# Kernel tuning notes

Measured on AMD Instinct MI355X. Metric: run time of the kernel, lower is better.

The kernel has to match this reference:

```python
import jax, jax.numpy as jnp
import numpy as np
import math
from jax import lax

D = 256      # d_model
H = 8        # heads
DK = D // H  # 32
P = 16       # patch size
IMG = 224
S = (IMG // P) ** 2 + 1  # 197
B = 64
EPS = 1e-5


def _ln(x, g, b):
    m = jnp.mean(x, axis=-1, keepdims=True)
    v = jnp.mean((x - m) ** 2, axis=-1, keepdims=True)
    return (x - m) / jnp.sqrt(v + EPS) * g + b


def _attn(q_in, k_in, v_in, wq, bq, wk, bk, wv, bv, wo, bo, mask):
    # torch Linear: y = x @ W^T + b
    def heads(x, w, b):
        y = x @ w.T + b
        bsz, s, _ = y.shape
        return y.reshape(bsz, s, H, DK).transpose(0, 2, 1, 3)  # [b,h,s,dk]
    q = heads(q_in, wq, bq)
    k = heads(k_in, wk, bk)
    v = heads(v_in, wv, bv)
    att = jnp.einsum('bhqd,bhkd->bhqk', q, k) / math.sqrt(DK)
    if mask is not None:
        att = jnp.where(mask == 0, -jnp.inf, att)
    att = jax.nn.softmax(att, axis=-1)
    o = jnp.einsum('bhqk,bhkd->bhqd', att, v)
    bsz, s, _ = q_in.shape  # output reshape uses q's shape (faithful to source)
    o = o.transpose(0, 2, 1, 3).reshape(bsz, s, D)
    return o @ wo.T + bo


def _patch_embed(img, conv_w, conv_b, cls, pos):
    x = lax.conv_general_dilated(img, conv_w, window_strides=(P, P),
                                 padding='VALID',
                                 dimension_numbers=('NCHW', 'OIHW', 'NCHW'))
    x = x + conv_b[None, :, None, None]
    bsz = img.shape[0]
    x = x.reshape(bsz, D, -1).transpose(0, 2, 1)  # [B,196,D]
    cls_t = jnp.broadcast_to(cls, (bsz, 1, D))
    x = jnp.concatenate([x, cls_t], axis=1)  # cls appended at END (faithful)
    return x + pos


def setup_inputs() -> dict:
    key = jax.random.key(0)
    ks = iter(jax.random.split(key, 64))
    nrm = lambda shape, s=0.02: jax.random.normal(next(ks), shape, jnp.float32) * s
    inp = {
        'enc_out': jax.random.normal(next(ks), (B, 3, IMG, IMG), jnp.float32),
        'dec_in': jax.random.normal(next(ks), (B, S, D), jnp.float32),
        'mask': jnp.ones((1, 1, S, S), jnp.int32),
        'conv_w': nrm((D, 3, P, P)),
        'conv_b': jnp.zeros((D,), jnp.float32),
        'cls': nrm((1, 1, D), 1.0),
        'pos': nrm((1, S, D), 1.0),
        'ff_w1': nrm((4 * D, D)), 'ff_b1': jnp.zeros((4 * D,), jnp.float32),
        'ff_w2': nrm((D, 4 * D)), 'ff_b2': jnp.zeros((D,), jnp.float32),
        'ln1_g': jnp.ones((D,), jnp.float32), 'ln1_b': jnp.zeros((D,), jnp.float32),
        'ln2_g': jnp.ones((D,), jnp.float32), 'ln2_b': jnp.zeros((D,), jnp.float32),
        'ln3_g': jnp.ones((D,), jnp.float32), 'ln3_b': jnp.zeros((D,), jnp.float32),
    }
    for p in ('a1', 'a2'):
        for n in ('wq', 'wk', 'wv', 'wo'):
            inp[f'{p}_{n}'] = nrm((D, D))
            inp[f'{p}_b{n[1]}'] = jnp.zeros((D,), jnp.float32)
    return inp


def reference(enc_out, dec_in, mask, conv_w, conv_b, cls, pos,
              ff_w1, ff_b1, ff_w2, ff_b2,
              ln1_g, ln1_b, ln2_g, ln2_b, ln3_g, ln3_b,
              a1_wq, a1_bq, a1_wk, a1_bk, a1_wv, a1_bv, a1_wo, a1_bo,
              a2_wq, a2_bq, a2_wk, a2_bk, a2_wv, a2_bv, a2_wo, a2_bo):
    e = _patch_embed(enc_out, conv_w, conv_b, cls, pos)  # [B,197,D]
    x = dec_in
    x = _ln(x + _attn(dec_in, dec_in, dec_in,
                      a1_wq, a1_bq, a1_wk, a1_bk, a1_wv, a1_bv, a1_wo, a1_bo,
                      None), ln1_g, ln1_b)
    # faithful: q=k=enc_out, v=dec_in, with mask
    x = _ln(x + _attn(e, e, dec_in,
                      a2_wq, a2_bq, a2_wk, a2_bk, a2_wv, a2_bv, a2_wo, a2_bo,
                      mask), ln2_g, ln2_b)
    ff = jax.nn.relu(x @ ff_w1.T + ff_b1) @ ff_w2.T + ff_b2
    x = _ln(x + ff, ln3_g, ln3_b)
    return x
```

## Files before the change

kernel.cpp:

```cpp
#include <hip/hip_runtime.h>
#include <hip/hip_bf16.h>
#include <math.h>

#define DMODEL 256
#define NH 8
#define DKH 32
#define SEQ 197
#define BATCH 64
#define NPAT 196
#define FFDIM 1024
#define KCONV 768
#define EPSLN 1e-5f
#define MROWS (BATCH * SEQ)
#define SP 224

typedef __attribute__((ext_vector_type(8))) short short8;
typedef __attribute__((ext_vector_type(4))) short short4v;
typedef __attribute__((ext_vector_type(4))) float floatx4;

__device__ inline short f2b(float f) {
  unsigned u = __float_as_uint(f);
  unsigned r = (u + 0x7FFFu + ((u >> 16) & 1u)) >> 16;
  return (short)r;
}
__device__ inline float b2f(short s) {
  return __uint_as_float(((unsigned)(unsigned short)s) << 16);
}

typedef const __attribute__((address_space(1))) unsigned int gu32;
typedef __attribute__((address_space(3))) unsigned int lu32;
__device__ __forceinline__ void gl_lds16(const void* g, void* l) {
  __builtin_amdgcn_global_load_lds((gu32*)g, (lu32*)l, 16, 0, 0);
}

__global__ __launch_bounds__(256) void convert_dec(
    const float* __restrict__ dec, short* __restrict__ dec_bf)
{
  const int ND = (MROWS * DMODEL) / 8;
  int i = blockIdx.x * 256 + threadIdx.x;
  if (i >= ND) return;
  float4 a0 = ((const float4*)dec)[i * 2];
  float4 a1 = ((const float4*)dec)[i * 2 + 1];
  short8 o;
  o[0] = f2b(a0.x); o[1] = f2b(a0.y); o[2] = f2b(a0.z); o[3] = f2b(a0.w);
  o[4] = f2b(a1.x); o[5] = f2b(a1.y); o[6] = f2b(a1.z); o[7] = f2b(a1.w);
  ((short8*)dec_bf)[i] = o;
}

__global__ __launch_bounds__(256) void prep_weights(
    const float* wq1, const float* wk1, const float* wv1,
    const float* bq1, const float* bk1, const float* bv1,
    const float* wq2, const float* wk2, const float* bq2, const float* bk2,
    const float* wv2s, const float* wo1, const float* wo2,
    const float* ffw1, const float* ffw2, const float* convw,
    short* Wqkv1, float* Bqkv1, short* Wqk2, float* Bqk2,
    short* Wv2, short* Wo1, short* Wo2, short* Wff1, short* Wff2, short* Wconv)
{
  int i = blockIdx.x * 256 + threadIdx.x;
  if (i < 65536) {
    Wqkv1[i] = f2b(wq1[i]); Wqkv1[65536 + i] = f2b(wk1[i]); Wqkv1[131072 + i] = f2b(wv1[i]);
    Wqk2[i] = f2b(wq2[i]);  Wqk2[65536 + i] = f2b(wk2[i]);
    Wv2[i] = f2b(wv2s[i]);  Wo1[i] = f2b(wo1[i]);  Wo2[i] = f2b(wo2[i]);
  }
  if (i < 262144) { Wff1[i] = f2b(ffw1[i]); Wff2[i] = f2b(ffw2[i]); }
  if (i < 196608) { Wconv[i] = f2b(convw[i]); }
  if (i < 256) {
    Bqkv1[i] = bq1[i]; Bqkv1[256 + i] = bk1[i]; Bqkv1[512 + i] = bv1[i];
    Bqk2[i] = bq2[i];  Bqk2[256 + i] = bk2[i];
  }
}

__global__ void mask_pack(const int* __restrict__ mask,
                          unsigned long long* __restrict__ bits,
                          unsigned long long* __restrict__ ones)
{
  int idx = blockIdx.x * 256 + threadIdx.x;
  if (idx >= SEQ * 4) return;
  int r = idx >> 2, w = idx & 3;
  unsigned long long bb = 0ull, oo = 0ull;
  for (int j = 0; j < 64; j++) {
    int c = w * 64 + j;
    if (c < SEQ) {
      oo |= (1ull << j);
      if (mask[r * SEQ + c] != 0) bb |= (1ull << j);
    }
  }
  bits[idx] = bb;
  ones[idx] = oo;
}

__global__ void cls_kernel(const float* __restrict__ cls, const float* __restrict__ pos,
                           short* __restrict__ e)
{
  int b = blockIdx.x, d = threadIdx.x;
  e[((size_t)b * SEQ + NPAT) * DMODEL + d] = f2b(cls[d] + pos[NPAT * DMODEL + d]);
}

__global__ __launch_bounds__(256) void gemm64(
    const short* __restrict__ A, const short* __restrict__ W,
    const float* __restrict__ bias, const short* __restrict__ res,
    float* __restrict__ outf, short* __restrict__ outb,
    int M, int N, int K, int relu)
{
  __shared__ short Al[64 * 64];
  __shared__ short Bl[64 * 64];
  int m0 = blockIdx.x * 64, n0 = blockIdx.y * 64;
  int t = threadIdx.x;
  int wave = t >> 6, lane = t & 63;
  int wm = (wave & 1) * 32, wn = (wave >> 1) * 32;
  int ml = lane & 15, quad = lane >> 4;
  int m7 = ml & 7;

  int rs = t >> 3;
  int cs = (t & 7) ^ (rs & 7);
  const short* gA0 = A + (size_t)(m0 + rs) * K + cs * 8;
  const short* gA1 = A + (size_t)(m0 + rs + 32) * K + cs * 8;
  const short* gB0 = W + (size_t)(n0 + rs) * K + cs * 8;
  const short* gB1 = W + (size_t)(n0 + rs + 32) * K + cs * 8;
  short* lA0 = &Al[t * 8];
  short* lA1 = &Al[t * 8 + 2048];
  short* lB0 = &Bl[t * 8];
  short* lB1 = &Bl[t * 8 + 2048];

  int offA[2][2], offB[2][2];
#pragma unroll
  for (int kk = 0; kk < 2; kk++)
#pragma unroll
    for (int i = 0; i < 2; i++) {
      int ra = wm + i * 16 + ml;
      offA[kk][i] = ra * 64 + (((kk * 4 + quad) ^ m7) * 8);
      int rb = wn + i * 16 + ml;
      offB[kk][i] = rb * 64 + (((kk * 4 + quad) ^ m7) * 8);
    }

  floatx4 z = {0.f, 0.f, 0.f, 0.f};
  floatx4 acc[2][2] = {{z, z}, {z, z}};

  for (int k0 = 0; k0 < K; k0 += 64) {
    __syncthreads();
    gl_lds16(gA0 + k0, lA0);
    gl_lds16(gA1 + k0, lA1);
    gl_lds16(gB0 + k0, lB0);
    gl_lds16(gB1 + k0, lB1);
    __builtin_amdgcn_s_waitcnt(0x0F70);
    __syncthreads();
#pragma unroll
    for (int kk = 0; kk < 2; kk++) {
      short8 a0 = *(const short8*)&Al[offA[kk][0]];
      short8 a1 = *(const short8*)&Al[offA[kk][1]];
      short8 b0 = *(const short8*)&Bl[offB[kk][0]];
      short8 b1 = *(const short8*)&Bl[offB[kk][1]];
      acc[0][0] = __builtin_amdgcn_mfma_f32_16x16x32_bf16(a0, b0, acc[0][0], 0, 0, 0);
      acc[0][1] = __builtin_amdgcn_mfma_f32_16x16x32_bf16(a0, b1, acc[0][1], 0, 0, 0);
      acc[1][0] = __builtin_amdgcn_mfma_f32_16x16x32_bf16(a1, b0, acc[1][0], 0, 0, 0);
      acc[1][1] = __builtin_amdgcn_mfma_f32_16x16x32_bf16(a1, b1, acc[1][1], 0, 0, 0);
    }
  }
#pragma unroll
  for (int i = 0; i < 2; i++)
#pragma unroll
    for (int j = 0; j < 2; j++)
#pragma unroll
      for (int rr = 0; rr < 4; rr++) {
        int row = m0 + wm + i * 16 + quad * 4 + rr;
        int col = n0 + wn + j * 16 + ml;
        float v = acc[i][j][rr] + bias[col];
        if (res) v += b2f(res[(size_t)row * N + col]);
        if (relu) v = fmaxf(v, 0.f);
        if (outf) outf[(size_t)row * N + col] = v;
        if (outb) outb[(size_t)row * N + col] = f2b(v);
      }
}

__global__ __launch_bounds__(256) void conv64(
    const float* __restrict__ img, const short* __restrict__ W,
    const float* __restrict__ cb, const float* __restrict__ pos,
    short* __restrict__ e)
{
  __shared__ short Al[64 * 64];
  __shared__ short Bl[64 * 64];
  int m0 = blockIdx.x * 64, n0 = blockIdx.y * 64;
  int t = threadIdx.x;
  int wave = t >> 6, lane = t & 63;
  int wm = (wave & 1) * 32, wn = (wave >> 1) * 32;
  int ml = lane & 15, quad = lane >> 4;
  int m7 = ml & 15 & 7;

  int rA = t >> 3, cg = t & 7;
  int pr_off = cg >> 1;
  int px_off = (cg & 1) * 8;
  int csw = cg ^ (rA & 7);
  const float* baseA[2];
  short* lA[2];
#pragma unroll
  for (int p = 0; p < 2; p++) {
    int m = m0 + rA + p * 32;
    int b = m / NPAT, pp = m - b * NPAT;
    int py = pp / 14, px = pp - py * 14;
    baseA[p] = img + (size_t)b * 3 * 50176 + (size_t)(py * 16) * 224 + px * 16 + px_off;
    lA[p] = &Al[(rA + p * 32) * 64 + csw * 8];
  }
  int rs = t >> 3;
  int cs = (t & 7) ^ (rs & 7);
  const short* gB0 = W + (size_t)(n0 + rs) * KCONV + cs * 8;
  const short* gB1 = W + (size_t)(n0 + rs + 32) * KCONV + cs * 8;
  short* lB0 = &Bl[t * 8];
  short* lB1 = &Bl[t * 8 + 2048];

  int offA[2][2], offB[2][2];
#pragma unroll
  for (int kk = 0; kk < 2; kk++)
#pragma unroll
    for (int i = 0; i < 2; i++) {
      int ra = wm + i * 16 + ml;
      offA[kk][i] = ra * 64 + (((kk * 4 + quad) ^ m7) * 8);
      int rb = wn + i * 16 + ml;
      offB[kk][i] = rb * 64 + (((kk * 4 + quad) ^ m7) * 8);
    }

  floatx4 z = {0.f, 0.f, 0.f, 0.f};
  floatx4 acc[2][2] = {{z, z}, {z, z}};

  for (int k0 = 0; k0 < KCONV; k0 += 64) {
    int ch = k0 >> 8;
    int rr0 = (k0 & 255) >> 4;
    __syncthreads();
    gl_lds16(gB0 + k0, lB0);
    gl_lds16(gB1 + k0, lB1);
#pragma unroll
    for (int p = 0; p < 2; p++) {
      const float* ap = baseA[p] + (size_t)ch * 50176 + (rr0 + pr_off) * 224;
      float4 a0 = *(const float4*)ap;
      float4 a1 = *(const float4*)(ap + 4);
      short8 av;
      av[0] = f2b(a0.x); av[1] = f2b(a0.y); av[2] = f2b(a0.z); av[3] = f2b(a0.w);
      av[4] = f2b(a1.x); av[5] = f2b(a1.y); av[6] = f2b(a1.z); av[7] = f2b(a1.w);
      *(short8*)lA[p] = av;
    }
    __builtin_amdgcn_s_waitcnt(0x0F70);
    __syncthreads();
#pragma unroll
    for (int kk = 0; kk < 2; kk++) {
      short8 a0 = *(const short8*)&Al[offA[kk][0]];
      short8 a1 = *(const short8*)&Al[offA[kk][1]];
      short8 b0 = *(const short8*)&Bl[offB[kk][0]];
      short8 b1 = *(const short8*)&Bl[offB[kk][1]];
      acc[0][0] = __builtin_amdgcn_mfma_f32_16x16x32_bf16(a0, b0, acc[0][0], 0, 0, 0);
      acc[0][1] = __builtin_amdgcn_mfma_f32_16x16x32_bf16(a0, b1, acc[0][1], 0, 0, 0);
      acc[1][0] = __builtin_amdgcn_mfma_f32_16x16x32_bf16(a1, b0, acc[1][0], 0, 0, 0);
      acc[1][1] = __builtin_amdgcn_mfma_f32_16x16x32_bf16(a1, b1, acc[1][1], 0, 0, 0);
    }
  }
#pragma unroll
  for (int i = 0; i < 2; i++)
#pragma unroll
    for (int j = 0; j < 2; j++)
#pragma unroll
      for (int rr = 0; rr < 4; rr++) {
        int mrow = m0 + wm + i * 16 + quad * 4 + rr;
        int b2 = mrow / NPAT, p2 = mrow - b2 * NPAT;
        int col = n0 + wn + j * 16 + ml;
        e[((size_t)b2 * SEQ + p2) * DMODEL + col] =
            f2b(acc[i][j][rr] + cb[col] + pos[p2 * DMODEL + col]);
      }
}

__global__ __launch_bounds__(256) void attn_mfma(
    const short* __restrict__ qp, int qstr,
    const short* __restrict__ kp, int kstr,
    const short* __restrict__ vp, int vstr,
    const unsigned long long* __restrict__ mbits,
    short* __restrict__ op)
{
  __shared__ short ks[SP][40];
  __shared__ short vt[DKH][SP + 8];
  __shared__ short ps[4][16][40];
  int bh = blockIdx.x;
  int b = bh >> 3, h = bh & 7;
  int t = threadIdx.x;
  int wave = t >> 6, lane = t & 63;
  int ml = lane & 15, quad = lane >> 4;

  const short* kb = kp + (size_t)b * SEQ * kstr + h * DKH;
  const short* vb = vp + (size_t)b * SEQ * vstr + h * DKH;
  for (int idx = t; idx < SEQ * 4; idx += 256) {
    int s = idx >> 2, c = (idx & 3) * 8;
    *(short8*)&ks[s][c] = *(const short8*)(kb + (size_t)s * kstr + c);
  }
  for (int idx = t; idx < SEQ * 4; idx += 256) {
    int s = idx >> 2, c = (idx & 3) * 8;
    short8 v8 = *(const short8*)(vb + (size_t)s * vstr + c);
#pragma unroll
    for (int j = 0; j < 8; j++) vt[c + j][s] = v8[j];
  }
  for (int idx = t; idx < DKH * (SP - SEQ); idx += 256) {
    int d = idx / (SP - SEQ), j = SEQ + idx - d * (SP - SEQ);
    vt[d][j] = 0;
  }
  __syncthreads();

  const float scale = 0.17677669529663687f;
  floatx4 z = {0.f, 0.f, 0.f, 0.f};

  for (int tt = 0; tt < 2; tt++) {
    int ti = blockIdx.y * 8 + wave * 2 + tt;
    int q0 = ti * 16;
    if (q0 >= SEQ) continue;
    int qrow = q0 + ml;
    int qc = qrow < SEQ ? qrow : SEQ - 1;
    short8 qf = *(const short8*)(qp + ((size_t)b * SEQ + qc) * qstr + h * DKH + quad * 8);
    const unsigned long long* mrow = mbits + (size_t)qc * 4;

    floatx4 accO0 = z, accO1 = z;
    float mrun = -1e30f, lrun = 0.f;

    for (int st = 0; st < 7; st++) {
      int j0 = st * 32;
      short8 k0 = *(const short8*)&ks[j0 + ml][quad * 8];
      short8 k1 = *(const short8*)&ks[j0 + 16 + ml][quad * 8];
      floatx4 s0 = __builtin_amdgcn_mfma_f32_16x16x32_bf16(k0, qf, z, 0, 0, 0);
      floatx4 s1 = __builtin_amdgcn_mfma_f32_16x16x32_bf16(k1, qf, z, 0, 0, 0);
      unsigned long long mb = mrow[j0 >> 6] >> (j0 & 63);
      float sv[8];
#pragma unroll
      for (int r = 0; r < 4; r++) {
        int jl = quad * 4 + r;
        sv[r]     = ((mb >> jl) & 1ull)        ? s0[r] * scale : -1e38f;
        sv[4 + r] = ((mb >> (16 + jl)) & 1ull) ? s1[r] * scale : -1e38f;
      }
      float tm = sv[0];
#pragma unroll
      for (int i = 1; i < 8; i++) tm = fmaxf(tm, sv[i]);
      tm = fmaxf(tm, __shfl_xor(tm, 16));
      tm = fmaxf(tm, __shfl_xor(tm, 32));
      float nm = fmaxf(mrun, tm);
      float alpha = __expf(mrun - nm);
      float pv[8];
      float psum = 0.f;
#pragma unroll
      for (int i = 0; i < 8; i++) { pv[i] = __expf(sv[i] - nm); psum += pv[i]; }
      psum += __shfl_xor(psum, 16);
      psum += __shfl_xor(psum, 32);
      lrun = lrun * alpha + psum;
      mrun = nm;
      accO0 = accO0 * alpha;
      accO1 = accO1 * alpha;
      short4v p0, p1;
#pragma unroll
      for (int r = 0; r < 4; r++) { p0[r] = f2b(pv[r]); p1[r] = f2b(pv[4 + r]); }
      *(short4v*)&ps[wave][ml][quad * 4]      = p0;
      *(short4v*)&ps[wave][ml][16 + quad * 4] = p1;
      __asm__ volatile("s_waitcnt lgkmcnt(0)" ::: "memory");
      short8 pf = *(const short8*)&ps[wave][ml][quad * 8];
      short8 vf0 = *(const short8*)&vt[ml][j0 + quad * 8];
      short8 vf1 = *(const short8*)&vt[16 + ml][j0 + quad * 8];
      accO0 = __builtin_amdgcn_mfma_f32_16x16x32_bf16(vf0, pf, accO0, 0, 0, 0);
      accO1 = __builtin_amdgcn_mfma_f32_16x16x32_bf16(vf1, pf, accO1, 0, 0, 0);
    }
    if (qrow < SEQ) {
      float inv = 1.f / lrun;
      short* ob = op + ((size_t)b * SEQ + qrow) * DMODEL + h * DKH;
      short4v o0, o1;
#pragma unroll
      for (int r = 0; r < 4; r++) {
        o0[r] = f2b(accO0[r] * inv);
        o1[r] = f2b(accO1[r] * inv);
      }
      *(short4v*)(ob + quad * 4)      = o0;
      *(short4v*)(ob + 16 + quad * 4) = o1;
    }
  }
}

__global__ __launch_bounds__(256) void ln_bf(
    const short* __restrict__ x, const float* __restrict__ g,
    const float* __restrict__ bt, float* __restrict__ outf,
    short* __restrict__ outb)
{
  int wave = threadIdx.x >> 6, lane = threadIdx.x & 63;
  int row = blockIdx.x * 4 + wave;
  short4v xv = *(const short4v*)(x + (size_t)row * DMODEL + lane * 4);
  float v0 = b2f(xv[0]), v1 = b2f(xv[1]), v2 = b2f(xv[2]), v3 = b2f(xv[3]);
  float s = v0 + v1 + v2 + v3;
  for (int off = 32; off; off >>= 1) s += __shfl_down(s, off);
  s = __shfl(s, 0);
  float mean = s * (1.0f / DMODEL);
  float d0 = v0 - mean, d1 = v1 - mean, d2 = v2 - mean, d3 = v3 - mean;
  float vv = d0 * d0 + d1 * d1 + d2 * d2 + d3 * d3;
  for (int off = 32; off; off >>= 1) vv += __shfl_down(vv, off);
  vv = __shfl(vv, 0);
  float inv = rsqrtf(vv * (1.0f / DMODEL) + EPSLN);
  float4 gg = *(const float4*)(g + lane * 4);
  float4 bb = *(const float4*)(bt + lane * 4);
  float r0 = d0 * inv * gg.x + bb.x;
  float r1 = d1 * inv * gg.y + bb.y;
  float r2 = d2 * inv * gg.z + bb.z;
  float r3 = d3 * inv * gg.w + bb.w;
  if (outf) {
    float4 o = {r0, r1, r2, r3};
    *(float4*)(outf + (size_t)row * DMODEL + lane * 4) = o;
  }
  if (outb) {
    short4v o;
    o[0] = f2b(r0); o[1] = f2b(r1); o[2] = f2b(r2); o[3] = f2b(r3);
    *(short4v*)(outb + (size_t)row * DMODEL + lane * 4) = o;
  }
}

extern "C" void kernel_launch(void* const* d_in, const int* in_sizes, int n_in,
                              void* d_out, int out_size, void* d_ws, size_t ws_size,
                              hipStream_t stream)
{
  const float* enc    = (const float*)d_in[0];
  const float* dec_in = (const float*)d_in[1];
  const int*   mask   = (const int*)  d_in[2];
  const float* conv_w = (const float*)d_in[3];
  const float* conv_b = (const float*)d_in[4];
  const float* cls    = (const float*)d_in[5];
  const float* pos    = (const float*)d_in[6];
  const float* ff_w1  = (const float*)d_in[7];
  const float* ff_b1  = (const float*)d_in[8];
  const float* ff_w2  = (const float*)d_in[9];
  const float* ff_b2  = (const float*)d_in[10];
  const float* ln1_g  = (const float*)d_in[11];
  const float* ln1_b  = (const float*)d_in[12];
  const float* ln2_g  = (const float*)d_in[13];
  const float* ln2_b  = (const float*)d_in[14];
  const float* ln3_g  = (const float*)d_in[15];
  const float* ln3_b  = (const float*)d_in[16];
  const float* a1_wq = (const float*)d_in[17]; const float* a1_bq = (const float*)d_in[18];
  const float* a1_wk = (const float*)d_in[19]; const float* a1_bk = (const float*)d_in[20];
  const float* a1_wv = (const float*)d_in[21]; const float* a1_bv = (const float*)d_in[22];
  const float* a1_wo = (const float*)d_in[23]; const float* a1_bo = (const float*)d_in[24];
  const float* a2_wq = (const float*)d_in[25]; const float* a2_bq = (const float*)d_in[26];
  const float* a2_wk = (const float*)d_in[27]; const float* a2_bk = (const float*)d_in[28];
  const float* a2_wv = (const float*)d_in[29]; const float* a2_bv = (const float*)d_in[30];
  const float* a2_wo = (const float*)d_in[31]; const float* a2_bo = (const float*)d_in[32];

  char* wsB = (char*)d_ws;
  short* Wqkv1 = (short*)wsB;
  short* Wqk2  = Wqkv1 + 196608;
  short* Wv2   = Wqk2 + 131072;
  short* Wo1   = Wv2 + 65536;
  short* Wo2   = Wo1 + 65536;
  short* Wff1  = Wo2 + 65536;
  short* Wff2  = Wff1 + 262144;
  short* Wconv = Wff2 + 262144;
  float* Bqkv1 = (float*)(Wconv + 196608);
  float* Bqk2  = Bqkv1 + 768;
  unsigned long long* mbits = (unsigned long long*)(Bqk2 + 512);
  unsigned long long* mones = mbits + 788;

  const size_t MB = 1048576;
  short* dec_bf = (short*)(wsB + 3 * MB);
  short* e_bf   = (short*)(wsB + 10 * MB);
  short* qkv1   = (short*)(wsB + 17 * MB);
  short* o1     = (short*)(wsB + 37 * MB);
  short* qk2    = (short*)(wsB + 44 * MB);
  short* v2     = (short*)(wsB + 57 * MB);
  short* h_buf  = (short*)(wsB + 64 * MB);
  short* t_bf   = (short*)(wsB + 90 * MB);
  short* x1b    = (short*)(wsB + 97 * MB);
  short* x2b    = (short*)(wsB + 104 * MB);
  short* o2     = o1;

  dim3 blk(256);
  const int M = MROWS;

  convert_dec<<<1576, blk, 0, stream>>>(dec_in, dec_bf);
  prep_weights<<<1024, blk, 0, stream>>>(
      a1_wq, a1_wk, a1_wv, a1_bq, a1_bk, a1_bv,
      a2_wq, a2_wk, a2_bq, a2_bk, a2_wv, a1_wo, a2_wo,
      ff_w1, ff_w2, conv_w,
      Wqkv1, Bqkv1, Wqk2, Bqk2, Wv2, Wo1, Wo2, Wff1, Wff2, Wconv);
  mask_pack<<<4, blk, 0, stream>>>(mask, mbits, mones);

  conv64<<<dim3(196, 4), blk, 0, stream>>>(enc, Wconv, conv_b, pos, e_bf);
  cls_kernel<<<BATCH, DMODEL, 0, stream>>>(cls, pos, e_bf);

  gemm64<<<dim3(197, 12), blk, 0, stream>>>(
      dec_bf, Wqkv1, Bqkv1, nullptr, nullptr, qkv1, M, 768, 256, 0);
  attn_mfma<<<dim3(512, 2), blk, 0, stream>>>(
      qkv1, 768, qkv1 + 256, 768, qkv1 + 512, 768, mones, o1);
  gemm64<<<dim3(197, 4), blk, 0, stream>>>(
      o1, Wo1, a1_bo, dec_bf, nullptr, t_bf, M, 256, 256, 0);
  ln_bf<<<M / 4, blk, 0, stream>>>(t_bf, ln1_g, ln1_b, nullptr, x1b);

  gemm64<<<dim3(197, 8), blk, 0, stream>>>(
      e_bf, Wqk2, Bqk2, nullptr, nullptr, qk2, M, 512, 256, 0);
  gemm64<<<dim3(197, 4), blk, 0, stream>>>(
      dec_bf, Wv2, a2_bv, nullptr, nullptr, v2, M, 256, 256, 0);
  attn_mfma<<<dim3(512, 2), blk, 0, stream>>>(
      qk2, 512, qk2 + 256, 512, v2, 256, mbits, o2);
  gemm64<<<dim3(197, 4), blk, 0, stream>>>(
      o2, Wo2, a2_bo, x1b, nullptr, t_bf, M, 256, 256, 0);
  ln_bf<<<M / 4, blk, 0, stream>>>(t_bf, ln2_g, ln2_b, nullptr, x2b);

  gemm64<<<dim3(197, 16), blk, 0, stream>>>(
      x2b, Wff1, ff_b1, nullptr, nullptr, h_buf, M, FFDIM, 256, 1);
  gemm64<<<dim3(197, 4), blk, 0, stream>>>(
      h_buf, Wff2, ff_b2, x2b, nullptr, t_bf, M, 256, 1024, 0);
  ln_bf<<<M / 4, blk, 0, stream>>>(t_bf, ln3_g, ln3_b, (float*)d_out, nullptr);
}
```

Before: 358.0 us.

## Merge independent kernels into phase launches and double-buffer GEMM LDS loads

Groups independent work (weight prep, mask pack, cls, dec conversion; conv with QKV and V2 GEMMs; attention1 with QK2 GEMM; Wo1 GEMM with attention2) into shared multi-role kernels dispatched by block index. This cuts the launch count from 17 to 11 and lets unrelated work fill the GPU at the same time. It also rewrites the GEMM main loop to double-buffer its LDS tiles with direct global-to-LDS loads, overlapping the next tile's fetch with the current MFMAs. The cost is a larger LDS footprint and register pressure in the merged kernels, which can lower occupancy.

Measured after the change: 333.8 us. -6.8%, faster.

```diff
diff --git a/kernel.cpp b/kernel.cpp
--- a/kernel.cpp
+++ b/kernel.cpp
@@ -33,94 +33,28 @@
   __builtin_amdgcn_global_load_lds((gu32*)g, (lu32*)l, 16, 0, 0);
 }
 
-__global__ __launch_bounds__(256) void convert_dec(
-    const float* __restrict__ dec, short* __restrict__ dec_bf)
-{
-  const int ND = (MROWS * DMODEL) / 8;
-  int i = blockIdx.x * 256 + threadIdx.x;
-  if (i >= ND) return;
-  float4 a0 = ((const float4*)dec)[i * 2];
-  float4 a1 = ((const float4*)dec)[i * 2 + 1];
-  short8 o;
-  o[0] = f2b(a0.x); o[1] = f2b(a0.y); o[2] = f2b(a0.z); o[3] = f2b(a0.w);
-  o[4] = f2b(a1.x); o[5] = f2b(a1.y); o[6] = f2b(a1.z); o[7] = f2b(a1.w);
-  ((short8*)dec_bf)[i] = o;
-}
-
-__global__ __launch_bounds__(256) void prep_weights(
-    const float* wq1, const float* wk1, const float* wv1,
-    const float* bq1, const float* bk1, const float* bv1,
-    const float* wq2, const float* wk2, const float* bq2, const float* bk2,
-    const float* wv2s, const float* wo1, const float* wo2,
-    const float* ffw1, const float* ffw2, const float* convw,
-    short* Wqkv1, float* Bqkv1, short* Wqk2, float* Bqk2,
-    short* Wv2, short* Wo1, short* Wo2, short* Wff1, short* Wff2, short* Wconv)
-{
-  int i = blockIdx.x * 256 + threadIdx.x;
-  if (i < 65536) {
-    Wqkv1[i] = f2b(wq1[i]); Wqkv1[65536 + i] = f2b(wk1[i]); Wqkv1[131072 + i] = f2b(wv1[i]);
-    Wqk2[i] = f2b(wq2[i]);  Wqk2[65536 + i] = f2b(wk2[i]);
-    Wv2[i] = f2b(wv2s[i]);  Wo1[i] = f2b(wo1[i]);  Wo2[i] = f2b(wo2[i]);
-  }
-  if (i < 262144) { Wff1[i] = f2b(ffw1[i]); Wff2[i] = f2b(ffw2[i]); }
-  if (i < 196608) { Wconv[i] = f2b(convw[i]); }
-  if (i < 256) {
-    Bqkv1[i] = bq1[i]; Bqkv1[256 + i] = bk1[i]; Bqkv1[512 + i] = bv1[i];
-    Bqk2[i] = bq2[i];  Bqk2[256 + i] = bk2[i];
-  }
-}
-
-__global__ void mask_pack(const int* __restrict__ mask,
-                          unsigned long long* __restrict__ bits,
-                          unsigned long long* __restrict__ ones)
-{
-  int idx = blockIdx.x * 256 + threadIdx.x;
-  if (idx >= SEQ * 4) return;
-  int r = idx >> 2, w = idx & 3;
-  unsigned long long bb = 0ull, oo = 0ull;
-  for (int j = 0; j < 64; j++) {
-    int c = w * 64 + j;
-    if (c < SEQ) {
-      oo |= (1ull << j);
-      if (mask[r * SEQ + c] != 0) bb |= (1ull << j);
-    }
-  }
-  bits[idx] = bb;
-  ones[idx] = oo;
-}
-
-__global__ void cls_kernel(const float* __restrict__ cls, const float* __restrict__ pos,
-                           short* __restrict__ e)
-{
-  int b = blockIdx.x, d = threadIdx.x;
-  e[((size_t)b * SEQ + NPAT) * DMODEL + d] = f2b(cls[d] + pos[NPAT * DMODEL + d]);
-}
-
-__global__ __launch_bounds__(256) void gemm64(
+__device__ __forceinline__ void gemm64_body(
+    char* smem, int bx, int by,
     const short* __restrict__ A, const short* __restrict__ W,
-    const float* __restrict__ bias, const short* __restrict__ res,
+    const float* __restrict__ bias, const short* __restrict__ resb,
     float* __restrict__ outf, short* __restrict__ outb,
-    int M, int N, int K, int relu)
-{
-  __shared__ short Al[64 * 64];
-  __shared__ short Bl[64 * 64];
-  int m0 = blockIdx.x * 64, n0 = blockIdx.y * 64;
-  int t = threadIdx.x;
-  int wave = t >> 6, lane = t & 63;
-  int wm = (wave & 1) * 32, wn = (wave >> 1) * 32;
-  int ml = lane & 15, quad = lane >> 4;
-  int m7 = ml & 7;
-
-  int rs = t >> 3;
-  int cs = (t & 7) ^ (rs & 7);
+    int N, int K, int relu)
+{
+  short* Al = (short*)smem;
+  short* Bl = (short*)(smem + 16384);
+  const int t = threadIdx.x;
+  const int wave = t >> 6, lane = t & 63;
+  const int wm = (wave & 1) * 32, wn = (wave >> 1) * 32;
+  const int ml = lane & 15, quad = lane >> 4;
+  const int m7 = ml & 7;
+  const int m0 = bx * 64, n0 = by * 64;
+
+  const int rs = t >> 3;
+  const int cs = (t & 7) ^ (rs & 7);
   const short* gA0 = A + (size_t)(m0 + rs) * K + cs * 8;
   const short* gA1 = A + (size_t)(m0 + rs + 32) * K + cs * 8;
   const short* gB0 = W + (size_t)(n0 + rs) * K + cs * 8;
   const short* gB1 = W + (size_t)(n0 + rs + 32) * K + cs * 8;
-  short* lA0 = &Al[t * 8];
-  short* lA1 = &Al[t * 8 + 2048];
-  short* lB0 = &Bl[t * 8];
-  short* lB1 = &Bl[t * 8 + 2048];
 
   int offA[2][2], offB[2][2];
 #pragma unroll
@@ -136,12 +70,120 @@
   floatx4 z = {0.f, 0.f, 0.f, 0.f};
   floatx4 acc[2][2] = {{z, z}, {z, z}};
 
-  for (int k0 = 0; k0 < K; k0 += 64) {
+  const int niter = K >> 6;
+  gl_lds16(gA0, Al + t * 8);
+  gl_lds16(gA1, Al + t * 8 + 2048);
+  gl_lds16(gB0, Bl + t * 8);
+  gl_lds16(gB1, Bl + t * 8 + 2048);
+  for (int k = 0; k < niter; k++) {
+    int cur = k & 1;
+    if (k + 1 < niter) {
+      int nb = (cur ^ 1) * 4096;
+      int k0 = (k + 1) << 6;
+      gl_lds16(gA0 + k0, Al + nb + t * 8);
+      gl_lds16(gA1 + k0, Al + nb + t * 8 + 2048);
+      gl_lds16(gB0 + k0, Bl + nb + t * 8);
+      gl_lds16(gB1 + k0, Bl + nb + t * 8 + 2048);
+      __builtin_amdgcn_s_waitcnt(0x0F74);
+    } else {
+      __builtin_amdgcn_s_waitcnt(0x0F70);
+    }
+    __asm__ volatile("s_barrier" ::: "memory");
+    const short* Ac = Al + cur * 4096;
+    const short* Bc = Bl + cur * 4096;
+#pragma unroll
+    for (int kk = 0; kk < 2; kk++) {
+      short8 a0 = *(const short8*)&Ac[offA[kk][0]];
+      short8 a1 = *(const short8*)&Ac[offA[kk][1]];
+      short8 b0 = *(const short8*)&Bc[offB[kk][0]];
+      short8 b1 = *(const short8*)&Bc[offB[kk][1]];
+      acc[0][0] = __builtin_amdgcn_mfma_f32_16x16x32_bf16(a0, b0, acc[0][0], 0, 0, 0);
+      acc[0][1] = __builtin_amdgcn_mfma_f32_16x16x32_bf16(a0, b1, acc[0][1], 0, 0, 0);
+      acc[1][0] = __builtin_amdgcn_mfma_f32_16x16x32_bf16(a1, b0, acc[1][0], 0, 0, 0);
+      acc[1][1] = __builtin_amdgcn_mfma_f32_16x16x32_bf16(a1, b1, acc[1][1], 0, 0, 0);
+    }
+    __asm__ volatile("s_barrier" ::: "memory");
+  }
+#pragma unroll
+  for (int i = 0; i < 2; i++)
+#pragma unroll
+    for (int j = 0; j < 2; j++)
+#pragma unroll
+      for (int rr = 0; rr < 4; rr++) {
+        int row = m0 + wm + i * 16 + quad * 4 + rr;
+        int col = n0 + wn + j * 16 + ml;
+        float v = acc[i][j][rr] + bias[col];
+        if (resb) v += b2f(resb[(size_t)row * N + col]);
+        if (relu) v = fmaxf(v, 0.f);
+        if (outf) outf[(size_t)row * N + col] = v;
+        if (outb) outb[(size_t)row * N + col] = f2b(v);
+      }
+}
+
+__device__ __forceinline__ void conv64_body(
+    char* smem, int bx, int by,
+    const float* __restrict__ img, const short* __restrict__ W,
+    const float* __restrict__ cb, const float* __restrict__ pos,
+    short* __restrict__ e)
+{
+  short* Al = (short*)smem;
+  short* Bl = (short*)(smem + 8192);
+  const int t = threadIdx.x;
+  const int wave = t >> 6, lane = t & 63;
+  const int wm = (wave & 1) * 32, wn = (wave >> 1) * 32;
+  const int ml = lane & 15, quad = lane >> 4;
+  const int m7 = ml & 7;
+  const int m0 = bx * 64, n0 = by * 64;
+
+  int rA = t >> 3, cg = t & 7;
+  int pr_off = cg >> 1;
+  int px_off = (cg & 1) * 8;
+  int csw = cg ^ (rA & 7);
+  const float* baseA[2];
+  short* lA[2];
+#pragma unroll
+  for (int p = 0; p < 2; p++) {
+    int m = m0 + rA + p * 32;
+    int b = m / NPAT, pp = m - b * NPAT;
+    int py = pp / 14, px = pp - py * 14;
+    baseA[p] = img + (size_t)b * 3 * 50176 + (size_t)(py * 16) * 224 + px * 16 + px_off;
+    lA[p] = &Al[(rA + p * 32) * 64 + csw * 8];
+  }
+  int rs = t >> 3;
+  int cs = (t & 7) ^ (rs & 7);
+  const short* gB0 = W + (size_t)(n0 + rs) * KCONV + cs * 8;
+  const short* gB1 = W + (size_t)(n0 + rs + 32) * KCONV + cs * 8;
+
+  int offA[2][2], offB[2][2];
+#pragma unroll
+  for (int kk = 0; kk < 2; kk++)
+#pragma unroll
+    for (int i = 0; i < 2; i++) {
+      int ra = wm + i * 16 + ml;
+      offA[kk][i] = ra * 64 + (((kk * 4 + quad) ^ m7) * 8);
+      int rb = wn + i * 16 + ml;
+      offB[kk][i] = rb * 64 + (((kk * 4 + quad) ^ m7) * 8);
+    }
+
+  floatx4 z = {0.f, 0.f, 0.f, 0.f};
+  floatx4 acc[2][2] = {{z, z}, {z, z}};
+
+  for (int k0 = 0; k0 < KCONV; k0 += 64) {
+    int ch = k0 >> 8;
+    int rr0 = (k0 & 255) >> 4;
     __syncthreads();
-    gl_lds16(gA0 + k0, lA0);
-    gl_lds16(gA1 + k0, lA1);
-    gl_lds16(gB0 + k0, lB0);
-    gl_lds16(gB1 + k0, lB1);
+    gl_lds16(gB0 + k0, Bl + t * 8);
+    gl_lds16(gB1 + k0, Bl + t * 8 + 2048);
+#pragma unroll
+    for (int p = 0; p < 2; p++) {
+      const float* ap = baseA[p] + (size_t)ch * 50176 + (rr0 + pr_off) * 224;
+      float4 a0 = *(const float4*)ap;
+      float4 a1 = *(const float4*)(ap + 4);
+      short8 av;
+      av[0] = f2b(a0.x); av[1] = f2b(a0.y); av[2] = f2b(a0.z); av[3] = f2b(a0.w);
+      av[4] = f2b(a1.x); av[5] = f2b(a1.y); av[6] = f2b(a1.z); av[7] = f2b(a1.w);
+      *(short8*)lA[p] = av;
+    }
     __builtin_amdgcn_s_waitcnt(0x0F70);
     __syncthreads();
 #pragma unroll
@@ -162,101 +204,6 @@
     for (int j = 0; j < 2; j++)
 #pragma unroll
       for (int rr = 0; rr < 4; rr++) {
-        int row = m0 + wm + i * 16 + quad * 4 + rr;
-        int col = n0 + wn + j * 16 + ml;
-        float v = acc[i][j][rr] + bias[col];
-        if (res) v += b2f(res[(size_t)row * N + col]);
-        if (relu) v = fmaxf(v, 0.f);
-        if (outf) outf[(size_t)row * N + col] = v;
-        if (outb) outb[(size_t)row * N + col] = f2b(v);
-      }
-}
-
-__global__ __launch_bounds__(256) void conv64(
-    const float* __restrict__ img, const short* __restrict__ W,
-    const float* __restrict__ cb, const float* __restrict__ pos,
-    short* __restrict__ e)
-{
-  __shared__ short Al[64 * 64];
-  __shared__ short Bl[64 * 64];
-  int m0 = blockIdx.x * 64, n0 = blockIdx.y * 64;
-  int t = threadIdx.x;
-  int wave = t >> 6, lane = t & 63;
-  int wm = (wave & 1) * 32, wn = (wave >> 1) * 32;
-  int ml = lane & 15, quad = lane >> 4;
-  int m7 = ml & 15 & 7;
-
-  int rA = t >> 3, cg = t & 7;
-  int pr_off = cg >> 1;
-  int px_off = (cg & 1) * 8;
-  int csw = cg ^ (rA & 7);
-  const float* baseA[2];
-  short* lA[2];
-#pragma unroll
-  for (int p = 0; p < 2; p++) {
-    int m = m0 + rA + p * 32;
-    int b = m / NPAT, pp = m - b * NPAT;
-    int py = pp / 14, px = pp - py * 14;
-    baseA[p] = img + (size_t)b * 3 * 50176 + (size_t)(py * 16) * 224 + px * 16 + px_off;
-    lA[p] = &Al[(rA + p * 32) * 64 + csw * 8];
-  }
-  int rs = t >> 3;
-  int cs = (t & 7) ^ (rs & 7);
-  const short* gB0 = W + (size_t)(n0 + rs) * KCONV + cs * 8;
-  const short* gB1 = W + (size_t)(n0 + rs + 32) * KCONV + cs * 8;
-  short* lB0 = &Bl[t * 8];
-  short* lB1 = &Bl[t * 8 + 2048];
-
-  int offA[2][2], offB[2][2];
-#pragma unroll
-  for (int kk = 0; kk < 2; kk++)
-#pragma unroll
-    for (int i = 0; i < 2; i++) {
-      int ra = wm + i * 16 + ml;
-      offA[kk][i] = ra * 64 + (((kk * 4 + quad) ^ m7) * 8);
-      int rb = wn + i * 16 + ml;
-      offB[kk][i] = rb * 64 + (((kk * 4 + quad) ^ m7) * 8);
-    }
-
-  floatx4 z = {0.f, 0.f, 0.f, 0.f};
-  floatx4 acc[2][2] = {{z, z}, {z, z}};
-
-  for (int k0 = 0; k0 < KCONV; k0 += 64) {
-    int ch = k0 >> 8;
-    int rr0 = (k0 & 255) >> 4;
-    __syncthreads();
-    gl_lds16(gB0 + k0, lB0);
-    gl_lds16(gB1 + k0, lB1);
-#pragma unroll
-    for (int p = 0; p < 2; p++) {
-      const float* ap = baseA[p] + (size_t)ch * 50176 + (rr0 + pr_off) * 224;
-      float4 a0 = *(const float4*)ap;
-      float4 a1 = *(const float4*)(ap + 4);
-      short8 av;
-      av[0] = f2b(a0.x); av[1] = f2b(a0.y); av[2] = f2b(a0.z); av[3] = f2b(a0.w);
-      av[4] = f2b(a1.x); av[5] = f2b(a1.y); av[6] = f2b(a1.z); av[7] = f2b(a1.w);
-      *(short8*)lA[p] = av;
-    }
-    __builtin_amdgcn_s_waitcnt(0x0F70);
-    __syncthreads();
-#pragma unroll
-    for (int kk = 0; kk < 2; kk++) {
-      short8 a0 = *(const short8*)&Al[offA[kk][0]];
-      short8 a1 = *(const short8*)&Al[offA[kk][1]];
-      short8 b0 = *(const short8*)&Bl[offB[kk][0]];
-      short8 b1 = *(const short8*)&Bl[offB[kk][1]];
-      acc[0][0] = __builtin_amdgcn_mfma_f32_16x16x32_bf16(a0, b0, acc[0][0], 0, 0, 0);
-      acc[0][1] = __builtin_amdgcn_mfma_f32_16x16x32_bf16(a0, b1, acc[0][1], 0, 0, 0);
-      acc[1][0] = __builtin_amdgcn_mfma_f32_16x16x32_bf16(a1, b0, acc[1][0], 0, 0, 0);
-      acc[1][1] = __builtin_amdgcn_mfma_f32_16x16x32_bf16(a1, b1, acc[1][1], 0, 0, 0);
-    }
-  }
-#pragma unroll
-  for (int i = 0; i < 2; i++)
-#pragma unroll
-    for (int j = 0; j < 2; j++)
-#pragma unroll
-      for (int rr = 0; rr < 4; rr++) {
         int mrow = m0 + wm + i * 16 + quad * 4 + rr;
         int b2 = mrow / NPAT, p2 = mrow - b2 * NPAT;
         int col = n0 + wn + j * 16 + ml;
@@ -265,21 +212,23 @@
       }
 }
 
-__global__ __launch_bounds__(256) void attn_mfma(
+__device__ __forceinline__ void attn_body(
+    char* smem, int bid2,
     const short* __restrict__ qp, int qstr,
     const short* __restrict__ kp, int kstr,
     const short* __restrict__ vp, int vstr,
     const unsigned long long* __restrict__ mbits,
     short* __restrict__ op)
 {
-  __shared__ short ks[SP][40];
-  __shared__ short vt[DKH][SP + 8];
-  __shared__ short ps[4][16][40];
-  int bh = blockIdx.x;
+  short (*ks)[40] = (short(*)[40])smem;
+  short (*vt)[SP + 8] = (short(*)[SP + 8])(smem + 17920);
+  short* psw = (short*)(smem + 32768);
+  int bh = bid2 >> 1, half = bid2 & 1;
   int b = bh >> 3, h = bh & 7;
   int t = threadIdx.x;
   int wave = t >> 6, lane = t & 63;
   int ml = lane & 15, quad = lane >> 4;
+  short* ps = psw + wave * 640;
 
   const short* kb = kp + (size_t)b * SEQ * kstr + h * DKH;
   const short* vb = vp + (size_t)b * SEQ * vstr + h * DKH;
@@ -303,7 +252,7 @@
   floatx4 z = {0.f, 0.f, 0.f, 0.f};
 
   for (int tt = 0; tt < 2; tt++) {
-    int ti = blockIdx.y * 8 + wave * 2 + tt;
+    int ti = half * 8 + wave * 2 + tt;
     int q0 = ti * 16;
     if (q0 >= SEQ) continue;
     int qrow = q0 + ml;
@@ -348,10 +297,10 @@
       short4v p0, p1;
 #pragma unroll
       for (int r = 0; r < 4; r++) { p0[r] = f2b(pv[r]); p1[r] = f2b(pv[4 + r]); }
-      *(short4v*)&ps[wave][ml][quad * 4]      = p0;
-      *(short4v*)&ps[wave][ml][16 + quad * 4] = p1;
+      *(short4v*)&ps[ml * 40 + quad * 4]      = p0;
+      *(short4v*)&ps[ml * 40 + 16 + quad * 4] = p1;
       __asm__ volatile("s_waitcnt lgkmcnt(0)" ::: "memory");
-      short8 pf = *(const short8*)&ps[wave][ml][quad * 8];
+      short8 pf = *(const short8*)&ps[ml * 40 + quad * 8];
       short8 vf0 = *(const short8*)&vt[ml][j0 + quad * 8];
       short8 vf1 = *(const short8*)&vt[16 + ml][j0 + quad * 8];
       accO0 = __builtin_amdgcn_mfma_f32_16x16x32_bf16(vf0, pf, accO0, 0, 0, 0);
@@ -370,6 +319,133 @@
       *(short4v*)(ob + 16 + quad * 4) = o1;
     }
   }
+}
+
+__global__ __launch_bounds__(256) void phase0(
+    const float* wq1, const float* wk1, const float* wv1,
+    const float* bq1, const float* bk1, const float* bv1,
+    const float* wq2, const float* wk2, const float* bq2, const float* bk2,
+    const float* wv2s, const float* wo1, const float* wo2,
+    const float* ffw1, const float* ffw2, const float* convw,
+    short* Wqkv1, float* Bqkv1, short* Wqk2, float* Bqk2,
+    short* Wv2, short* Wo1, short* Wo2, short* Wff1, short* Wff2, short* Wconv,
+    const int* mask, unsigned long long* bits, unsigned long long* ones,
+    const float* cls, const float* pos, short* e,
+    const float* dec, short* dec_bf)
+{
+  int bid = blockIdx.x;
+  int t = threadIdx.x;
+  if (bid < 1024) {
+    int i = bid * 256 + t;
+    if (i < 65536) {
+      Wqkv1[i] = f2b(wq1[i]); Wqkv1[65536 + i] = f2b(wk1[i]); Wqkv1[131072 + i] = f2b(wv1[i]);
+      Wqk2[i] = f2b(wq2[i]);  Wqk2[65536 + i] = f2b(wk2[i]);
+      Wv2[i] = f2b(wv2s[i]);  Wo1[i] = f2b(wo1[i]);  Wo2[i] = f2b(wo2[i]);
+    }
+    Wff1[i] = f2b(ffw1[i]); Wff2[i] = f2b(ffw2[i]);
+    if (i < 196608) Wconv[i] = f2b(convw[i]);
+    if (i < 256) {
+      Bqkv1[i] = bq1[i]; Bqkv1[256 + i] = bk1[i]; Bqkv1[512 + i] = bv1[i];
+      Bqk2[i] = bq2[i];  Bqk2[256 + i] = bk2[i];
+    }
+  } else if (bid < 1028) {
+    int idx = (bid - 1024) * 256 + t;
+    if (idx < SEQ * 4) {
+      int r = idx >> 2, w = idx & 3;
+      unsigned long long bb = 0ull, oo = 0ull;
+      for (int j = 0; j < 64; j++) {
+        int c = w * 64 + j;
+        if (c < SEQ) {
+          oo |= (1ull << j);
+          if (mask[r * SEQ + c] != 0) bb |= (1ull << j);
+        }
+      }
+      bits[idx] = bb;
+      ones[idx] = oo;
+    }
+  } else if (bid < 1092) {
+    int b = bid - 1028, d = t;
+    e[((size_t)b * SEQ + NPAT) * DMODEL + d] = f2b(cls[d] + pos[NPAT * DMODEL + d]);
+  } else {
+    const int ND = (MROWS * DMODEL) / 8;
+    int i = (bid - 1092) * 256 + t;
+    if (i < ND) {
+      float4 a0 = ((const float4*)dec)[i * 2];
+      float4 a1 = ((const float4*)dec)[i * 2 + 1];
+      short8 o;
+      o[0] = f2b(a0.x); o[1] = f2b(a0.y); o[2] = f2b(a0.z); o[3] = f2b(a0.w);
+      o[4] = f2b(a1.x); o[5] = f2b(a1.y); o[6] = f2b(a1.z); o[7] = f2b(a1.w);
+      ((short8*)dec_bf)[i] = o;
+    }
+  }
+}
+
+__global__ __launch_bounds__(256) void phase1(
+    const float* __restrict__ enc, const short* __restrict__ Wconv,
+    const float* __restrict__ conv_b, const float* __restrict__ pos,
+    short* __restrict__ e_bf,
+    const short* __restrict__ dec_bf,
+    const short* __restrict__ Wqkv1, const float* __restrict__ Bqkv1,
+    short* __restrict__ qkv1,
+    const short* __restrict__ Wv2, const float* __restrict__ bv2,
+    short* __restrict__ v2)
+{
+  __shared__ char smem[32768];
+  int bid = blockIdx.x;
+  if (bid < 784) {
+    conv64_body(smem, bid % 196, bid / 196, enc, Wconv, conv_b, pos, e_bf);
+  } else if (bid < 3148) {
+    int idx = bid - 784;
+    gemm64_body(smem, idx % 197, idx / 197, dec_bf, Wqkv1, Bqkv1, nullptr,
+                nullptr, qkv1, 768, 256, 0);
+  } else {
+    int idx = bid - 3148;
+    gemm64_body(smem, idx % 197, idx / 197, dec_bf, Wv2, bv2, nullptr,
+                nullptr, v2, 256, 256, 0);
+  }
+}
+
+__global__ __launch_bounds__(256) void phase2(
+    const short* __restrict__ qkv1, const unsigned long long* __restrict__ mones,
+    short* __restrict__ o1,
+    const short* __restrict__ e_bf, const short* __restrict__ Wqk2,
+    const float* __restrict__ Bqk2, short* __restrict__ qk2)
+{
+  __shared__ char smem[37888];
+  int bid = blockIdx.x;
+  if (bid < 1024) {
+    attn_body(smem, bid, qkv1, 768, qkv1 + 256, 768, qkv1 + 512, 768, mones, o1);
+  } else {
+    int idx = bid - 1024;
+    gemm64_body(smem, idx % 197, idx / 197, e_bf, Wqk2, Bqk2, nullptr,
+                nullptr, qk2, 512, 256, 0);
+  }
+}
+
+__global__ __launch_bounds__(256) void phase3(
+    const short* __restrict__ o1, const short* __restrict__ Wo1,
+    const float* __restrict__ bo1, const short* __restrict__ dec_bf,
+    short* __restrict__ t_bf,
+    const short* __restrict__ qk2, const short* __restrict__ v2,
+    const unsigned long long* __restrict__ mbits, short* __restrict__ o2)
+{
+  __shared__ char smem[37888];
+  int bid = blockIdx.x;
+  if (bid < 788) {
+    gemm64_body(smem, bid % 197, bid / 197, o1, Wo1, bo1, dec_bf,
+                nullptr, t_bf, 256, 256, 0);
+  } else {
+    attn_body(smem, bid - 788, qk2, 512, qk2 + 256, 512, v2, 256, mbits, o2);
+  }
+}
+
+__global__ __launch_bounds__(256) void gemm_k(
+    const short* __restrict__ A, const short* __restrict__ W,
+    const float* __restrict__ bias, const short* __restrict__ resb,
+    float* __restrict__ outf, short* __restrict__ outb, int N, int K, int relu)
+{
+  __shared__ char smem[32768];
+  gemm64_body(smem, blockIdx.x, blockIdx.y, A, W, bias, resb, outf, outb, N, K, relu);
 }
 
 __global__ __launch_bounds__(256) void ln_bf(
@@ -467,38 +543,35 @@
   dim3 blk(256);
   const int M = MROWS;
 
-  convert_dec<<<1576, blk, 0, stream>>>(dec_in, dec_bf);
-  prep_weights<<<1024, blk, 0, stream>>>(
+  phase0<<<2668, blk, 0, stream>>>(
       a1_wq, a1_wk, a1_wv, a1_bq, a1_bk, a1_bv,
       a2_wq, a2_wk, a2_bq, a2_bk, a2_wv, a1_wo, a2_wo,
       ff_w1, ff_w2, conv_w,
-      Wqkv1, Bqkv1, Wqk2, Bqk2, Wv2, Wo1, Wo2, Wff1, Wff2, Wconv);
-  mask_pack<<<4, blk, 0, stream>>>(mask, mbits, mones);
-
-  conv64<<<dim3(196, 4), blk, 0, stream>>>(enc, Wconv, conv_b, pos, e_bf);
-  cls_kernel<<<BATCH, DMODEL, 0, stream>>>(cls, pos, e_bf);
-
-  gemm64<<<dim3(197, 12), blk, 0, stream>>>(
-      dec_bf, Wqkv1, Bqkv1, nullptr, nullptr, qkv1, M, 768, 256, 0);
-  attn_mfma<<<dim3(512, 2), blk, 0, stream>>>(
-      qkv1, 768, qkv1 + 256, 768, qkv1 + 512, 768, mones, o1);
-  gemm64<<<dim3(197, 4), blk, 0, stream>>>(
-      o1, Wo1, a1_bo, dec_bf, nullptr, t_bf, M, 256, 256, 0);
+      Wqkv1, Bqkv1, Wqk2, Bqk2, Wv2, Wo1, Wo2, Wff1, Wff2, Wconv,
+      mask, mbits, mones, cls, pos, e_bf, dec_in, dec_bf);
+
+  phase1<<<3936, blk, 0, stream>>>(
+      enc, Wconv, conv_b, pos, e_bf,
+      dec_bf, Wqkv1, Bqkv1, qkv1, Wv2, a2_bv, v2);
+
+  phase2<<<2600, blk, 0, stream>>>(
+      qkv1, mones, o1, e_bf, Wqk2, Bqk2, qk2);
+
+  phase3<<<1812, blk, 0, stream>>>(
+      o1, Wo1, a1_bo, dec_bf, t_bf, qk2, v2, mbits, o2);
+
   ln_bf<<<M / 4, blk, 0, stream>>>(t_bf, ln1_g, ln1_b, nullptr, x1b);
 
-  gemm64<<<dim3(197, 8), blk, 0, stream>>>(
-      e_bf, Wqk2, Bqk2, nullptr, nullptr, qk2, M, 512, 256, 0);
-  gemm64<<<dim3(197, 4), blk, 0, stream>>>(
-      dec_bf, Wv2, a2_bv, nullptr, nullptr, v2, M, 256, 256, 0);
-  attn_mfma<<<dim3(512, 2), blk, 0, stream>>>(
-      qk2, 512, qk2 + 256, 512, v2, 256, mbits, o2);
-  gemm64<<<dim3(197, 4), blk, 0, stream>>>(
-      o2, Wo2, a2_bo, x1b, nullptr, t_bf, M, 256, 256, 0);
+  gemm_k<<<dim3(197, 4), blk, 0, stream>>>(
+      o2, Wo2, a2_bo, x1b, nullptr, t_bf, 256, 256, 0);
+
   ln_bf<<<M / 4, blk, 0, stream>>>(t_bf, ln2_g, ln2_b, nullptr, x2b);
 
-  gemm64<<<dim3(197, 16), blk, 0, stream>>>(
-      x2b, Wff1, ff_b1, nullptr, nullptr, h_buf, M, FFDIM, 256, 1);
-  gemm64<<<dim3(197, 4), blk, 0, stream>>>(
-      h_buf, Wff2, ff_b2, x2b, nullptr, t_bf, M, 256, 1024, 0);
+  gemm_k<<<dim3(197, 16), blk, 0, stream>>>(
+      x2b, Wff1, ff_b1, nullptr, nullptr, h_buf, FFDIM, 256, 1);
+
+  gemm_k<<<dim3(197, 4), blk, 0, stream>>>(
+      h_buf, Wff2, ff_b2, x2b, nullptr, t_bf, 256, 1024, 0);
+
   ln_bf<<<M / 4, blk, 0, stream>>>(t_bf, ln3_g, ln3_b, (float*)d_out, nullptr);
 }
```
